# Optimization experiments

Measured on AMD Instinct MI355X. Metric: run time of the kernel, lower is better.

## Reference

```python
import jax, jax.numpy as jnp
import numpy as np

# static config matching init_kwargs
NODE, K, KER, STR = 32, 10, 5, 2
B, C = 8, 64
N = NODE * NODE          # 1024 nodes per sample
BN = B * N               # 8192 total nodes
OUT = (NODE - KER) // STR + 1
E = OUT * OUT            # local hyperedges per sample (196)
BN_EPS = 1e-5


def _local_block_diag():
    """Static block-diagonal local incidence matrix (BN, B*E), built once in numpy."""
    idx = np.arange(N).reshape(NODE, NODE)
    H_local = np.zeros((N, E), np.float32)
    e = 0
    for i in range(0, NODE - KER + 1, STR):
        for j in range(0, NODE - KER + 1, STR):
            H_local[idx[i:i + KER, j:j + KER].ravel(), e] = 1.0
            e += 1
    blk = np.zeros((BN, B * E), np.float32)
    for b in range(B):
        blk[b * N:(b + 1) * N, b * E:(b + 1) * E] = H_local
    return jnp.asarray(blk)


_LOCAL_BLK = _local_block_diag()


def setup_inputs() -> dict:
    key = jax.random.key(0)
    k1, k2 = jax.random.split(key, 2)
    x = jax.random.normal(k1, (B, N, C), jnp.float32)
    W_conv = jax.random.normal(k2, (C, C), jnp.float32) * 0.05
    b_conv = jnp.zeros((C,), jnp.float32)
    gamma = jnp.ones((C,), jnp.float32)
    beta = jnp.zeros((C,), jnp.float32)
    return {"x": x, "W_conv": W_conv, "b_conv": b_conv, "gamma": gamma, "beta": beta}


def reference(x, W_conv, b_conv, gamma, beta):
    xm = x.reshape(BN, C)                       # merged nodes (B*N, C)

    # --- hypergraph construction (no_grad in torch) ---
    xs = jax.lax.stop_gradient(xm)
    sq = jnp.sum(xs * xs, axis=-1, keepdims=True)
    dists = sq - 2.0 * (xs @ xs.T) + sq.T       # (BN, BN) pairwise sq-dists
    _, inds = jax.lax.top_k(-dists, K + 1)      # K+1 smallest distances
    # weights_function(prob=False) -> all ones; scatter incidence
    H = jnp.zeros((BN, BN), x.dtype).at[jnp.arange(BN)[:, None], inds].set(1.0)
    # Dv == K+1 for every row -> max_k = K+1 and the second topk gives new_H == H
    Hfull = jnp.concatenate([H, _LOCAL_BLK], axis=1)  # (BN, BN + B*E)

    # G = Dv^{-1/2} H W De^{-1} H^T Dv^{-1/2}, W = I, via diagonal scaling
    DV = Hfull.sum(axis=1)
    DE = jnp.maximum(Hfull.sum(axis=0), 1e-8)
    dv2 = DV ** -0.5
    A = dv2[:, None] * Hfull
    G = (A * (1.0 / DE)[None, :]) @ A.T          # (BN, BN)
    G = jax.lax.stop_gradient(G)

    # --- HGNN conv: linear -> G matmul -> BN (train stats) -> relu -> residual ---
    y = xm @ W_conv.T + b_conv                   # (BN, C)
    z = G @ y                                    # (BN, C)
    mu = z.mean(axis=0)
    var = z.var(axis=0)                          # biased, as torch BN training
    zn = (z - mu) / jnp.sqrt(var + BN_EPS) * gamma + beta
    out = jax.nn.relu(zn) + xm
    return out.reshape(B, N, C)
```

## Files before the change

kernel.cpp:

```cpp
#include <hip/hip_runtime.h>
#include <math.h>

#define BNTOT 8192
#define CH    64
#define KP1   11
#define NLOC  1568
#define MARGIN 1.0f
#define LCAPR 512

typedef __attribute__((ext_vector_type(8))) short short8;
typedef __attribute__((ext_vector_type(4))) float float4v;

__device__ __forceinline__ int pcnt(int p) {
  int lo = p - 4; if (lo < 0) lo = 0; lo += (lo & 1);
  int hi = p; if (hi > 26) hi = 26;
  return (hi >= lo) ? (((hi - lo) >> 1) + 1) : 0;
}
__device__ __forceinline__ float dv2_of(int u) {
  int node = u & 1023;
  int rr = node >> 5, cc = node & 31;
  int dv = KP1 + pcnt(rr) * pcnt(cc);
  return 1.0f / sqrtf((float)dv);
}
__device__ __forceinline__ unsigned short f2bf(float f) {
  unsigned u = __float_as_uint(f);
  unsigned r = (u + 0x7FFFu + ((u >> 16) & 1u)) >> 16;
  return (unsigned short)r;
}
__device__ __forceinline__ unsigned fkey(float s) {
  unsigned u = __float_as_uint(s);
  return (u & 0x80000000u) ? ~u : (u | 0x80000000u);
}
__device__ __forceinline__ unsigned long long skey(float s, int idx) {
  return ((unsigned long long)fkey(s) << 32) | (unsigned)idx;
}
__device__ __forceinline__ int mbcnt64(unsigned long long m) {
  return __builtin_amdgcn_mbcnt_hi((unsigned)(m >> 32),
         __builtin_amdgcn_mbcnt_lo((unsigned)m, 0));
}
__device__ __forceinline__ int wave_count4(int l) {
  return     __popcll(__ballot(l & 1))
       + 2 * __popcll(__ballot(l & 2))
       + 4 * __popcll(__ballot(l & 4))
       + 8 * __popcll(__ballot(l & 8));
}

__global__ void k_cast(const float* __restrict__ X, unsigned short* __restrict__ Xh,
                       float* __restrict__ sq) {
  int g = blockIdx.x * 256 + threadIdx.x;
  int lane = threadIdx.x & 63;
  float v = X[g];
  Xh[g] = f2bf(v);
  float s = v * v;
  #pragma unroll
  for (int off = 32; off >= 1; off >>= 1) s += __shfl_xor(s, off, 64);
  if (lane == 0) sq[g >> 6] = s;
}

__global__ __launch_bounds__(256)
void k_thrpart(const float* __restrict__ X, const float* __restrict__ sq,
               float* __restrict__ part) {
  const int tid = threadIdx.x, wave = tid >> 6, lane = tid & 63;
  const int rg = blockIdx.x >> 3, chunk = blockIdx.x & 7;
  const int row = rg * 64 + lane;
  float xr[CH];
  {
    const float4* xp = (const float4*)(X + (size_t)row * CH);
    #pragma unroll
    for (int k = 0; k < CH / 4; ++k) {
      float4 v = xp[k];
      xr[4*k+0] = v.x; xr[4*k+1] = v.y; xr[4*k+2] = v.z; xr[4*k+3] = v.w;
    }
  }
  float tv[KP1];
  #pragma unroll
  for (int t = 0; t < KP1; ++t) tv[t] = INFINITY;

  for (int s = 0; s < 32; ++s) {
    int j = __builtin_amdgcn_readfirstlane(((chunk * 4 + wave) * 32 + s) * 8);
    const float* cp = X + (size_t)j * CH;
    float d0 = 0.f, d1 = 0.f, d2 = 0.f, d3 = 0.f;
    #pragma unroll
    for (int k = 0; k < CH / 4; ++k) {
      d0 = fmaf(xr[4*k+0], cp[4*k+0], d0);
      d1 = fmaf(xr[4*k+1], cp[4*k+1], d1);
      d2 = fmaf(xr[4*k+2], cp[4*k+2], d2);
      d3 = fmaf(xr[4*k+3], cp[4*k+3], d3);
    }
    float cv = fmaf(-2.0f, (d0 + d1) + (d2 + d3), sq[j]);
    #pragma unroll
    for (int t = 0; t < KP1; ++t) {
      float lo = fminf(tv[t], cv), hi = fmaxf(tv[t], cv);
      tv[t] = lo; cv = hi;
    }
  }
  __shared__ float ls[4][64][KP1];
  #pragma unroll
  for (int t = 0; t < KP1; ++t) ls[wave][lane][t] = tv[t];
  __syncthreads();
  if (tid < 64) {
    float v[KP1];
    #pragma unroll
    for (int t = 0; t < KP1; ++t) v[t] = ls[0][tid][t];
    #pragma unroll
    for (int w = 1; w < 4; ++w)
      #pragma unroll
      for (int t = 0; t < KP1; ++t) {
        float cv = ls[w][tid][t];
        #pragma unroll
        for (int s2 = 0; s2 < KP1; ++s2) {
          float lo = fminf(v[s2], cv), hi = fmaxf(v[s2], cv);
          v[s2] = lo; cv = hi;
        }
      }
    size_t base = ((size_t)blockIdx.x * 64 + tid) * KP1;
    #pragma unroll
    for (int t = 0; t < KP1; ++t) part[base + t] = v[t];
  }
}

__global__ void k_thrmerge(const float* __restrict__ part, float* __restrict__ thr) {
  const int rg = blockIdx.x, lane = threadIdx.x;
  const int row = rg * 64 + lane;
  float v[KP1];
  {
    size_t b0 = ((size_t)(rg * 8) * 64 + lane) * KP1;
    #pragma unroll
    for (int t = 0; t < KP1; ++t) v[t] = part[b0 + t];
  }
  for (int c = 1; c < 8; ++c) {
    size_t b = ((size_t)(rg * 8 + c) * 64 + lane) * KP1;
    #pragma unroll
    for (int t = 0; t < KP1; ++t) {
      float cv = part[b + t];
      #pragma unroll
      for (int s2 = 0; s2 < KP1; ++s2) {
        float lo = fminf(v[s2], cv), hi = fmaxf(v[s2], cv);
        v[s2] = lo; cv = hi;
      }
    }
  }
  thr[row] = v[KP1 - 1] + MARGIN;
}

__global__ __launch_bounds__(256)
void k_filter(const unsigned short* __restrict__ Xh, const float* __restrict__ sq,
              const float* __restrict__ thr, unsigned long long* __restrict__ mask) {
  const int tid = threadIdx.x, wave = tid >> 6, lane = tid & 63;
  const int m = lane & 15, q = lane >> 4;
  const int rowbase = (blockIdx.x >> 5) * 64;
  const int colbase = (blockIdx.x & 31) * 256 + wave * 64;
  const int wcol = (blockIdx.x & 31) * 4 + wave;

  short8 a[4][2];
  #pragma unroll
  for (int rt = 0; rt < 4; ++rt)
    #pragma unroll
    for (int kc = 0; kc < 2; ++kc)
      a[rt][kc] = *(const short8*)(Xh + (size_t)(rowbase + rt * 16 + m) * CH + kc * 32 + q * 8);

  short8 b0[4], b1[4];
  float sqv[4];
  #pragma unroll
  for (int sub = 0; sub < 4; ++sub) {
    const int coln = colbase + sub * 16 + m;
    const short8* bp = (const short8*)(Xh + (size_t)coln * CH + q * 8);
    b0[sub] = bp[0];
    b1[sub] = bp[4];
    sqv[sub] = sq[coln];
  }

  float thrv[16];
  #pragma unroll
  for (int rt = 0; rt < 4; ++rt)
    #pragma unroll
    for (int r = 0; r < 4; ++r)
      thrv[rt * 4 + r] = thr[rowbase + rt * 16 + q * 4 + r];

  const float4v cz = {0.f, 0.f, 0.f, 0.f};
  const int sr = lane & 15, qq = sr >> 2, rr = sr & 3;

  #pragma unroll
  for (int rt = 0; rt < 4; ++rt) {
    unsigned long long bal[4][4];
    #pragma unroll
    for (int sub = 0; sub < 4; ++sub) {
      float4v c = __builtin_amdgcn_mfma_f32_16x16x32_bf16(a[rt][0], b0[sub], cz, 0, 0, 0);
      c = __builtin_amdgcn_mfma_f32_16x16x32_bf16(a[rt][1], b1[sub], c, 0, 0, 0);
      #pragma unroll
      for (int r = 0; r < 4; ++r) {
        float score = fmaf(-2.0f, c[r], sqv[sub]);
        bal[sub][r] = __ballot(score < thrv[rt * 4 + r]);
      }
    }
    unsigned long long w = 0;
    #pragma unroll
    for (int sub = 0; sub < 4; ++sub) {
      unsigned long long bsel = (rr == 0) ? bal[sub][0]
                              : (rr == 1) ? bal[sub][1]
                              : (rr == 2) ? bal[sub][2]
                              :             bal[sub][3];
      unsigned long long slice = (bsel >> (qq * 16)) & 0xFFFFull;
      w |= slice << (sub * 16);
    }
    if ((lane >> 4) == rt)
      mask[(size_t)(rowbase + rt * 16 + sr) * 128 + wcol] = w;
  }
}

__global__ __launch_bounds__(256)
void k_rescore(const float* __restrict__ X, const float* __restrict__ sq,
               const unsigned long long* __restrict__ mask,
               int* __restrict__ inds, int* __restrict__ DE) {
  __shared__ int cols[4][LCAPR];
  const int tid = threadIdx.x, lane = tid & 63, wv = tid >> 6;
  const int row = __builtin_amdgcn_readfirstlane(blockIdx.x * 4 + wv);

  float xr[CH];
  {
    const float4* xp = (const float4*)(X + (size_t)row * CH);
    #pragma unroll
    for (int k = 0; k < CH / 4; ++k) {
      float4 v = xp[k];
      xr[4*k+0] = v.x; xr[4*k+1] = v.y; xr[4*k+2] = v.z; xr[4*k+3] = v.w;
    }
  }

  const unsigned long long* mrow = mask + (size_t)row * 128;
  unsigned long long w0 = mrow[lane * 2 + 0];
  unsigned long long w1 = mrow[lane * 2 + 1];

  int cnt = __popcll(w0) + __popcll(w1);
  int p = 0, total = 0;
  #pragma unroll
  for (int b = 0; b < 8; ++b) {
    unsigned long long bb = __ballot((cnt >> b) & 1);
    p     += mbcnt64(bb) << b;
    total += __popcll(bb) << b;
  }

  if (total <= LCAPR) {
    unsigned long long w = w0;
    while (w) { int b = __builtin_ctzll(w); w &= w - 1; cols[wv][p++] = lane * 128 + b; }
    w = w1;
    while (w) { int b = __builtin_ctzll(w); w &= w - 1; cols[wv][p++] = lane * 128 + 64 + b; }

    unsigned kscore[8]; int kidx[8];
    #pragma unroll
    for (int a = 0; a < 8; ++a) { kscore[a] = 0xFFFFFFFFu; kidx[a] = 0; }
    #pragma unroll
    for (int a = 0; a < 8; ++a) {
      int s = a * 64 + lane;
      bool valid = s < total;
      int cj = cols[wv][valid ? s : 0];
      const float4* cp = (const float4*)(X + (size_t)cj * CH);
      float d0 = 0.f, d1 = 0.f, d2 = 0.f, d3 = 0.f;
      #pragma unroll
      for (int k = 0; k < CH / 4; ++k) {
        float4 v = cp[k];
        d0 = fmaf(xr[4*k+0], v.x, d0);
        d1 = fmaf(xr[4*k+1], v.y, d1);
        d2 = fmaf(xr[4*k+2], v.z, d2);
        d3 = fmaf(xr[4*k+3], v.w, d3);
      }
      float score = fmaf(-2.0f, (d0 + d1) + (d2 + d3), sq[cj]);
      if (valid) { kscore[a] = fkey(score); kidx[a] = cj; }
    }

    unsigned long long blo = 0, bhi = 1ull << 32;
    for (int it = 0; it < 32; ++it) {
      unsigned mid = (unsigned)((blo + bhi) >> 1);
      int l = 0;
      #pragma unroll
      for (int a = 0; a < 8; ++a) l += (kscore[a] < mid);
      if (wave_count4(l) < KP1) blo = mid; else bhi = mid;
    }
    const unsigned T = (unsigned)blo;

    int ll = 0, le = 0;
    #pragma unroll
    for (int a = 0; a < 8; ++a) { ll += (kscore[a] < T); le += (kscore[a] <= T); }
    int c_less = wave_count4(ll);
    int c_le   = wave_count4(le);
    const int needed = KP1 - c_less;
    const int cnt_eq = c_le - c_less;

    unsigned idxcut = BNTOT;
    if (cnt_eq != needed) {
      int lo2 = 0, hi2 = BNTOT;
      for (int it = 0; it < 13; ++it) {
        int mid2 = (lo2 + hi2) >> 1;
        int l2 = 0;
        #pragma unroll
        for (int a = 0; a < 8; ++a) l2 += ((kscore[a] == T) & (kidx[a] < mid2));
        if (wave_count4(l2) < needed) lo2 = mid2; else hi2 = mid2;
      }
      idxcut = (unsigned)hi2;
    }

    int base = 0;
    #pragma unroll
    for (int a = 0; a < 8; ++a) {
      bool win = (kscore[a] < T) | ((kscore[a] == T) & ((unsigned)kidx[a] < idxcut));
      unsigned long long bal = __ballot(win);
      int pos = base + mbcnt64(bal);
      if (win) {
        inds[(size_t)row * KP1 + pos] = kidx[a];
        atomicAdd(&DE[kidx[a]], 1);
      }
      base += __popcll(bal);
    }
  } else {
    float tv[KP1]; int ti[KP1];
    #pragma unroll
    for (int t = 0; t < KP1; ++t) { tv[t] = INFINITY; ti[t] = -1; }
    for (int s = lane; s < BNTOT; s += 64) {
      const float4* cp = (const float4*)(X + (size_t)s * CH);
      float d0 = 0.f, d1 = 0.f, d2 = 0.f, d3 = 0.f;
      #pragma unroll
      for (int k = 0; k < CH / 4; ++k) {
        float4 v = cp[k];
        d0 = fmaf(xr[4*k+0], v.x, d0);
        d1 = fmaf(xr[4*k+1], v.y, d1);
        d2 = fmaf(xr[4*k+2], v.z, d2);
        d3 = fmaf(xr[4*k+3], v.w, d3);
      }
      float score = fmaf(-2.0f, (d0 + d1) + (d2 + d3), sq[s]);
      if (score < tv[KP1 - 1]) {
        float cv = score; int ci = s;
        #pragma unroll
        for (int t = 0; t < KP1; ++t) {
          bool sw = cv < tv[t];
          float nv = sw ? cv    : tv[t]; int ni = sw ? ci    : ti[t];
          float ov = sw ? tv[t] : cv;    int oi = sw ? ti[t] : ci;
          tv[t] = nv; ti[t] = ni; cv = ov; ci = oi;
        }
      }
    }
    unsigned long long cur = skey(tv[0], ti[0]);
    unsigned long long keep = 0;
    #pragma unroll
    for (int t = 0; t < KP1; ++t) {
      unsigned long long mw = cur;
      #pragma unroll
      for (int off = 1; off < 64; off <<= 1) {
        unsigned lo = __shfl_xor((unsigned)mw, off, 64);
        unsigned hi = __shfl_xor((unsigned)(mw >> 32), off, 64);
        unsigned long long o = ((unsigned long long)hi << 32) | lo;
        mw = (o < mw) ? o : mw;
      }
      if (lane == t) keep = mw;
      if (cur == mw) {
        #pragma unroll
        for (int q = 0; q < KP1 - 1; ++q) { tv[q] = tv[q+1]; ti[q] = ti[q+1]; }
        tv[KP1-1] = INFINITY; ti[KP1-1] = -1;
        cur = skey(tv[0], ti[0]);
      }
    }
    if (lane < KP1) {
      int idx = (int)(unsigned)(keep & 0xFFFFFFFFull);
      inds[(size_t)row * KP1 + lane] = idx;
      atomicAdd(&DE[idx], 1);
    }
  }
}

__global__ void k_lin(const float* __restrict__ X, const float* __restrict__ W,
                      const float* __restrict__ bias, float* __restrict__ t) {
  int lane = threadIdx.x & 63;
  int wave = threadIdx.x >> 6;
  int rowbase = (blockIdx.x * 4 + wave) * 4;
  float wr[CH];
  {
    const float4* wp = (const float4*)(W + (size_t)lane * CH);
    #pragma unroll
    for (int k = 0; k < CH / 4; ++k) {
      float4 v = wp[k];
      wr[4*k+0] = v.x; wr[4*k+1] = v.y; wr[4*k+2] = v.z; wr[4*k+3] = v.w;
    }
  }
  float bc = bias[lane];
  #pragma unroll
  for (int r = 0; r < 4; ++r) {
    int row = __builtin_amdgcn_readfirstlane(rowbase + r);
    const float* xp = X + (size_t)row * CH;
    float d0 = 0.f, d1 = 0.f, d2 = 0.f, d3 = 0.f;
    #pragma unroll
    for (int k = 0; k < CH / 4; ++k) {
      d0 = fmaf(wr[4*k+0], xp[4*k+0], d0);
      d1 = fmaf(wr[4*k+1], xp[4*k+1], d1);
      d2 = fmaf(wr[4*k+2], xp[4*k+2], d2);
      d3 = fmaf(wr[4*k+3], xp[4*k+3], d3);
    }
    float y = (d0 + d1) + (d2 + d3) + bc;
    t[(size_t)row * CH + lane] = y * dv2_of(row);
  }
}

__global__ void k_edge(const float* __restrict__ t, const int* __restrict__ inds,
                       float* __restrict__ s_knn, float* __restrict__ s_loc) {
  int c = threadIdx.x & 63;
  int w = threadIdx.x >> 6;
  if (blockIdx.x < BNTOT / 4) {
    int u = blockIdx.x * 4 + w;
    float val = t[(size_t)u * CH + c];
    int ub = __builtin_amdgcn_readfirstlane(u);
    const int* ip = inds + (size_t)ub * KP1;
    #pragma unroll
    for (int j = 0; j < KP1; ++j) {
      int e = ip[j];
      atomicAdd(&s_knn[(size_t)e * CH + c], val);
    }
  } else {
    int e = (blockIdx.x - BNTOT / 4) * 4 + w;
    int b  = e / 196;
    int le = e - b * 196;
    int pi = le / 14;
    int pj = le - pi * 14;
    int base = b * 1024 + (pi * 2) * 32 + pj * 2;
    float acc = 0.f;
    #pragma unroll
    for (int di = 0; di < 5; ++di)
      #pragma unroll
      for (int dj = 0; dj < 5; ++dj)
        acc += t[(size_t)(base + di * 32 + dj) * CH + c];
    s_loc[(size_t)e * CH + c] = acc * (1.0f / 25.0f);
  }
}

__global__ void k_gatherbn(const float* __restrict__ s_knn, const float* __restrict__ s_loc,
                           const int* __restrict__ inds, const int* __restrict__ DE,
                           float* __restrict__ z, float* __restrict__ gsum,
                           float* __restrict__ gsumsq) {
  int c = threadIdx.x & 63;
  int w = threadIdx.x >> 6;
  int u = blockIdx.x * 4 + w;
  int ub = __builtin_amdgcn_readfirstlane(u);
  const int* ip = inds + (size_t)ub * KP1;
  float acc = 0.f;
  #pragma unroll
  for (int j = 0; j < KP1; ++j) {
    int e = ip[j];
    float invde = 1.0f / (float)DE[e];
    acc += s_knn[(size_t)e * CH + c] * invde;
  }
  int node = ub & 1023, b = ub >> 10;
  int rr = node >> 5, cc = node & 31;
  int i0 = rr - 4; if (i0 < 0) i0 = 0; i0 += (i0 & 1);
  int i1 = rr; if (i1 > 26) i1 = 26;
  int j0 = cc - 4; if (j0 < 0) j0 = 0; j0 += (j0 & 1);
  int j1 = cc; if (j1 > 26) j1 = 26;
  for (int i = i0; i <= i1; i += 2)
    for (int jj = j0; jj <= j1; jj += 2) {
      int e = b * 196 + (i >> 1) * 14 + (jj >> 1);
      acc += s_loc[(size_t)e * CH + c];
    }
  float zv = acc * dv2_of(ub);
  z[(size_t)ub * CH + c] = zv;

  __shared__ float ls[4][CH], ls2[4][CH];
  ls[w][c] = zv; ls2[w][c] = zv * zv;
  __syncthreads();
  if (threadIdx.x < 64) {
    int bin = (blockIdx.x & 7) * CH;
    atomicAdd(&gsum[bin + c],   ls[0][c] + ls[1][c] + ls[2][c] + ls[3][c]);
    atomicAdd(&gsumsq[bin + c], ls2[0][c] + ls2[1][c] + ls2[2][c] + ls2[3][c]);
  }
}

__global__ void k_out(const float* __restrict__ z, const float* __restrict__ X,
                      const float* __restrict__ gsum, const float* __restrict__ gsumsq,
                      const float* __restrict__ gamma, const float* __restrict__ beta,
                      float* __restrict__ out) {
  int c = threadIdx.x & 63;
  int w = threadIdx.x >> 6;
  float S = 0.f, S2 = 0.f;
  #pragma unroll
  for (int b = 0; b < 8; ++b) {
    S  += gsum[b * CH + c];
    S2 += gsumsq[b * CH + c];
  }
  float m = S * (1.0f / (float)BNTOT);
  float var = S2 * (1.0f / (float)BNTOT) - m * m;
  float rstd = 1.0f / sqrtf(var + 1e-5f);

  int u = blockIdx.x * 4 + w;
  size_t idx = (size_t)u * CH + c;
  float zn = (z[idx] - m) * rstd * gamma[c] + beta[c];
  out[idx] = fmaxf(zn, 0.f) + X[idx];
}

extern "C" void kernel_launch(void* const* d_in, const int* in_sizes, int n_in,
                              void* d_out, int out_size, void* d_ws, size_t ws_size,
                              hipStream_t stream) {
  const float* X     = (const float*)d_in[0];
  const float* W     = (const float*)d_in[1];
  const float* bias  = (const float*)d_in[2];
  const float* gamma = (const float*)d_in[3];
  const float* beta  = (const float*)d_in[4];
  float* out = (float*)d_out;

  float* ws = (float*)d_ws;
  float* sq      = ws;
  float* thr     = sq + 8192;
  float* t       = thr + 8192;
  float* s_loc   = t + 524288;
  float* z       = s_loc + 100352;
  float* thrpart = z + 524288;
  int*   inds    = (int*)(thrpart + 720896);
  unsigned short* Xh = (unsigned short*)(inds + 90112);
  unsigned long long* mask = (unsigned long long*)(Xh + 524288);
  int*   DE     = (int*)(mask + (size_t)8192 * 128);
  float* gsum   = (float*)(DE + 8192);
  float* gsumsq = gsum + 512;
  float* s_knn  = gsumsq + 512;

  hipMemsetAsync(DE, 0, (size_t)(8192 + 512 + 512 + 524288) * 4, stream);

  k_cast    <<<2048, 256, 0, stream>>>(X, Xh, sq);
  k_thrpart <<<1024, 256, 0, stream>>>(X, sq, thrpart);
  k_thrmerge<<<128, 64, 0, stream>>>(thrpart, thr);
  k_filter  <<<4096, 256, 0, stream>>>(Xh, sq, thr, mask);
  k_rescore <<<2048, 256, 0, stream>>>(X, sq, mask, inds, DE);
  k_lin     <<<512, 256, 0, stream>>>(X, W, bias, t);
  k_edge    <<<BNTOT / 4 + NLOC / 4, 256, 0, stream>>>(t, inds, s_knn, s_loc);
  k_gatherbn<<<BNTOT / 4, 256, 0, stream>>>(s_knn, s_loc, inds, DE, z, gsum, gsumsq);
  k_out     <<<BNTOT / 4, 256, 0, stream>>>(z, X, gsum, gsumsq, gamma, beta, out);

  (void)in_sizes; (void)n_in; (void)out_size; (void)ws_size;
}
```

Before: 240.5 us.

## Rescore candidates with 16-lane cooperative dot products and DPP reductions

The fast path of the rescoring kernel no longer has each lane compute a full 64-channel dot product against its own candidate from a 64-float register copy of the query row. Each group of 16 lanes now loads coalesced float4 slices, and cross-lane DPP adds reduce the partial sums, so four candidates are scored per step. This cuts register pressure and spreads memory access across lanes. The candidate cap drops from 512 to 256, and the full-row fallback (now holding the query in registers only there) handles more rows, which costs more if many rows exceed 256 candidates.

```diff
diff --git a/kernel.cpp b/kernel.cpp
--- a/kernel.cpp
+++ b/kernel.cpp
@@ -6,7 +6,7 @@
 #define KP1   11
 #define NLOC  1568
 #define MARGIN 1.0f
-#define LCAPR 512
+#define LCAPR 256
 
 typedef __attribute__((ext_vector_type(8))) short short8;
 typedef __attribute__((ext_vector_type(4))) float float4v;
@@ -43,6 +43,11 @@
        + 2 * __popcll(__ballot(l & 2))
        + 4 * __popcll(__ballot(l & 4))
        + 8 * __popcll(__ballot(l & 8));
+}
+template <int CTRL>
+__device__ __forceinline__ float dpp_add(float x) {
+  int p = __builtin_amdgcn_update_dpp(0, __float_as_int(x), CTRL, 0xF, 0xF, true);
+  return x + __int_as_float(p);
 }
 
 __global__ void k_cast(const float* __restrict__ X, unsigned short* __restrict__ Xh,
@@ -214,17 +219,7 @@
                int* __restrict__ inds, int* __restrict__ DE) {
   __shared__ int cols[4][LCAPR];
   const int tid = threadIdx.x, lane = tid & 63, wv = tid >> 6;
-  const int row = __builtin_amdgcn_readfirstlane(blockIdx.x * 4 + wv);
-
-  float xr[CH];
-  {
-    const float4* xp = (const float4*)(X + (size_t)row * CH);
-    #pragma unroll
-    for (int k = 0; k < CH / 4; ++k) {
-      float4 v = xp[k];
-      xr[4*k+0] = v.x; xr[4*k+1] = v.y; xr[4*k+2] = v.z; xr[4*k+3] = v.w;
-    }
-  }
+  const int row = __builtin_amdgcn_readfirstlane(blockIdx.x * 4 + (tid >> 6));
 
   const unsigned long long* mrow = mask + (size_t)row * 128;
   unsigned long long w0 = mrow[lane * 2 + 0];
@@ -245,26 +240,32 @@
     w = w1;
     while (w) { int b = __builtin_ctzll(w); w &= w - 1; cols[wv][p++] = lane * 128 + 64 + b; }
 
-    unsigned kscore[8]; int kidx[8];
-    #pragma unroll
-    for (int a = 0; a < 8; ++a) { kscore[a] = 0xFFFFFFFFu; kidx[a] = 0; }
-    #pragma unroll
-    for (int a = 0; a < 8; ++a) {
-      int s = a * 64 + lane;
-      bool valid = s < total;
-      int cj = cols[wv][valid ? s : 0];
-      const float4* cp = (const float4*)(X + (size_t)cj * CH);
-      float d0 = 0.f, d1 = 0.f, d2 = 0.f, d3 = 0.f;
-      #pragma unroll
-      for (int k = 0; k < CH / 4; ++k) {
-        float4 v = cp[k];
-        d0 = fmaf(xr[4*k+0], v.x, d0);
-        d1 = fmaf(xr[4*k+1], v.y, d1);
-        d2 = fmaf(xr[4*k+2], v.z, d2);
-        d3 = fmaf(xr[4*k+3], v.w, d3);
-      }
-      float score = fmaf(-2.0f, (d0 + d1) + (d2 + d3), sq[cj]);
-      if (valid) { kscore[a] = fkey(score); kidx[a] = cj; }
+    const int m = lane & 15, q = lane >> 4;
+    const float4 xrv = *(const float4*)(X + (size_t)row * CH + m * 4);
+
+    unsigned kscore[4]; int kidx[4];
+    #pragma unroll
+    for (int a = 0; a < 4; ++a) { kscore[a] = 0xFFFFFFFFu; kidx[a] = 0; }
+
+    #pragma unroll
+    for (int slot = 0; slot < 4; ++slot) {
+      if (slot * 64 < total) {
+        #pragma unroll
+        for (int b = 0; b < 16; ++b) {
+          int s = slot * 64 + b * 4 + q;
+          bool valid = s < total;
+          int sc = valid ? s : (total - 1);
+          int cj = cols[wv][sc];
+          const float4 v = *(const float4*)(X + (size_t)cj * CH + m * 4);
+          float d = fmaf(xrv.x, v.x, fmaf(xrv.y, v.y, fmaf(xrv.z, v.z, xrv.w * v.w)));
+          d = dpp_add<0xB1>(d);
+          d = dpp_add<0x4E>(d);
+          d = dpp_add<0x141>(d);
+          d = dpp_add<0x140>(d);
+          float score = fmaf(-2.0f, d, sq[cj]);
+          if (valid && m == b) { kscore[slot] = fkey(score); kidx[slot] = cj; }
+        }
+      }
     }
 
     unsigned long long blo = 0, bhi = 1ull << 32;
@@ -272,14 +273,14 @@
       unsigned mid = (unsigned)((blo + bhi) >> 1);
       int l = 0;
       #pragma unroll
-      for (int a = 0; a < 8; ++a) l += (kscore[a] < mid);
+      for (int a = 0; a < 4; ++a) l += (kscore[a] < mid);
       if (wave_count4(l) < KP1) blo = mid; else bhi = mid;
     }
     const unsigned T = (unsigned)blo;
 
     int ll = 0, le = 0;
     #pragma unroll
-    for (int a = 0; a < 8; ++a) { ll += (kscore[a] < T); le += (kscore[a] <= T); }
+    for (int a = 0; a < 4; ++a) { ll += (kscore[a] < T); le += (kscore[a] <= T); }
     int c_less = wave_count4(ll);
     int c_le   = wave_count4(le);
     const int needed = KP1 - c_less;
@@ -292,7 +293,7 @@
         int mid2 = (lo2 + hi2) >> 1;
         int l2 = 0;
         #pragma unroll
-        for (int a = 0; a < 8; ++a) l2 += ((kscore[a] == T) & (kidx[a] < mid2));
+        for (int a = 0; a < 4; ++a) l2 += ((kscore[a] == T) & (kidx[a] < mid2));
         if (wave_count4(l2) < needed) lo2 = mid2; else hi2 = mid2;
       }
       idxcut = (unsigned)hi2;
@@ -300,7 +301,7 @@
 
     int base = 0;
     #pragma unroll
-    for (int a = 0; a < 8; ++a) {
+    for (int a = 0; a < 4; ++a) {
       bool win = (kscore[a] < T) | ((kscore[a] == T) & ((unsigned)kidx[a] < idxcut));
       unsigned long long bal = __ballot(win);
       int pos = base + mbcnt64(bal);
@@ -311,6 +312,15 @@
       base += __popcll(bal);
     }
   } else {
+    float xr[CH];
+    {
+      const float4* xp = (const float4*)(X + (size_t)row * CH);
+      #pragma unroll
+      for (int k = 0; k < CH / 4; ++k) {
+        float4 v = xp[k];
+        xr[4*k+0] = v.x; xr[4*k+1] = v.y; xr[4*k+2] = v.z; xr[4*k+3] = v.w;
+      }
+    }
     float tv[KP1]; int ti[KP1];
     #pragma unroll
     for (int t = 0; t < KP1; ++t) { tv[t] = INFINITY; ti[t] = -1; }
@@ -352,7 +362,7 @@
       if (lane == t) keep = mw;
       if (cur == mw) {
         #pragma unroll
-        for (int q = 0; q < KP1 - 1; ++q) { tv[q] = tv[q+1]; ti[q] = ti[q+1]; }
+        for (int q2 = 0; q2 < KP1 - 1; ++q2) { tv[q2] = tv[q2+1]; ti[q2] = ti[q2+1]; }
         tv[KP1-1] = INFINITY; ti[KP1-1] = -1;
         cur = skey(tv[0], ti[0]);
       }
```

After: 250.6 us. 4.2% more time.

## Split each rescore row across four waves and merge per-wave top-K in shared memory

Applied to the files above, without the earlier changes.

k_rescore now assigns one block per row, with each of the four waves handling a quarter of the candidate bitmask (2048 columns). Each wave selects its local top-11 by a threshold binary search, writes the keys to shared memory, and wave 0 then merges the 44 candidates to the final top-11. The goal is to raise parallelism and cut the per-wave serial work (fewer candidate slots per lane, and a per-quarter fallback scan instead of a full 8192-column scan). The cost is four times as many blocks, a block-wide barrier and an extra merge step, and the per-wave capacity is lower (128), so the slow fallback path may trigger more often.

```diff
diff --git a/kernel.cpp b/kernel.cpp
--- a/kernel.cpp
+++ b/kernel.cpp
@@ -6,7 +6,7 @@
 #define KP1   11
 #define NLOC  1568
 #define MARGIN 1.0f
-#define LCAPR 512
+#define LCAPW 128
 
 typedef __attribute__((ext_vector_type(8))) short short8;
 typedef __attribute__((ext_vector_type(4))) float float4v;
@@ -31,12 +31,13 @@
   unsigned u = __float_as_uint(s);
   return (u & 0x80000000u) ? ~u : (u | 0x80000000u);
 }
-__device__ __forceinline__ unsigned long long skey(float s, int idx) {
-  return ((unsigned long long)fkey(s) << 32) | (unsigned)idx;
-}
 __device__ __forceinline__ int mbcnt64(unsigned long long m) {
   return __builtin_amdgcn_mbcnt_hi((unsigned)(m >> 32),
          __builtin_amdgcn_mbcnt_lo((unsigned)m, 0));
+}
+__device__ __forceinline__ int wave_count2(int l) {
+  return     __popcll(__ballot(l & 1))
+       + 2 * __popcll(__ballot(l & 2));
 }
 __device__ __forceinline__ int wave_count4(int l) {
   return     __popcll(__ballot(l & 1))
@@ -210,11 +211,12 @@
 
 __global__ __launch_bounds__(256)
 void k_rescore(const float* __restrict__ X, const float* __restrict__ sq,
-               const unsigned long long* __restrict__ mask,
+               const unsigned* __restrict__ mask32,
                int* __restrict__ inds, int* __restrict__ DE) {
-  __shared__ int cols[4][LCAPR];
+  __shared__ int cols[4][LCAPW];
+  __shared__ unsigned long long wkeys[4 * KP1];
   const int tid = threadIdx.x, lane = tid & 63, wv = tid >> 6;
-  const int row = __builtin_amdgcn_readfirstlane(blockIdx.x * 4 + wv);
+  const int row = blockIdx.x;
 
   float xr[CH];
   {
@@ -226,95 +228,80 @@
     }
   }
 
-  const unsigned long long* mrow = mask + (size_t)row * 128;
-  unsigned long long w0 = mrow[lane * 2 + 0];
-  unsigned long long w1 = mrow[lane * 2 + 1];
-
-  int cnt = __popcll(w0) + __popcll(w1);
-  int p = 0, total = 0;
-  #pragma unroll
-  for (int b = 0; b < 8; ++b) {
+  unsigned wbits = mask32[(size_t)row * 256 + wv * 64 + lane];
+  int cnt = __popc(wbits);
+  int p = 0, subtotal = 0;
+  #pragma unroll
+  for (int b = 0; b < 6; ++b) {
     unsigned long long bb = __ballot((cnt >> b) & 1);
-    p     += mbcnt64(bb) << b;
-    total += __popcll(bb) << b;
-  }
-
-  if (total <= LCAPR) {
-    unsigned long long w = w0;
-    while (w) { int b = __builtin_ctzll(w); w &= w - 1; cols[wv][p++] = lane * 128 + b; }
-    w = w1;
-    while (w) { int b = __builtin_ctzll(w); w &= w - 1; cols[wv][p++] = lane * 128 + 64 + b; }
-
-    unsigned kscore[8]; int kidx[8];
-    #pragma unroll
-    for (int a = 0; a < 8; ++a) { kscore[a] = 0xFFFFFFFFu; kidx[a] = 0; }
-    #pragma unroll
-    for (int a = 0; a < 8; ++a) {
-      int s = a * 64 + lane;
-      bool valid = s < total;
-      int cj = cols[wv][valid ? s : 0];
-      const float4* cp = (const float4*)(X + (size_t)cj * CH);
-      float d0 = 0.f, d1 = 0.f, d2 = 0.f, d3 = 0.f;
-      #pragma unroll
-      for (int k = 0; k < CH / 4; ++k) {
-        float4 v = cp[k];
-        d0 = fmaf(xr[4*k+0], v.x, d0);
-        d1 = fmaf(xr[4*k+1], v.y, d1);
-        d2 = fmaf(xr[4*k+2], v.z, d2);
-        d3 = fmaf(xr[4*k+3], v.w, d3);
-      }
-      float score = fmaf(-2.0f, (d0 + d1) + (d2 + d3), sq[cj]);
-      if (valid) { kscore[a] = fkey(score); kidx[a] = cj; }
+    p        += mbcnt64(bb) << b;
+    subtotal += __popcll(bb) << b;
+  }
+
+  if (subtotal <= LCAPW) {
+    const int cbase = wv * 2048 + lane * 32;
+    unsigned w = wbits;
+    while (w) { int b = __builtin_ctz(w); w &= w - 1; cols[wv][p++] = cbase + b; }
+
+    unsigned ks[2]; int ki[2];
+    ks[0] = ks[1] = 0xFFFFFFFFu; ki[0] = lane; ki[1] = 64 + lane;
+    #pragma unroll
+    for (int a = 0; a < 2; ++a) {
+      if (a * 64 < subtotal) {
+        int s = a * 64 + lane;
+        bool valid = s < subtotal;
+        int cj = cols[wv][valid ? s : (subtotal - 1)];
+        const float4* cp = (const float4*)(X + (size_t)cj * CH);
+        float d0 = 0.f, d1 = 0.f, d2 = 0.f, d3 = 0.f;
+        #pragma unroll
+        for (int k = 0; k < CH / 4; ++k) {
+          float4 v = cp[k];
+          d0 = fmaf(xr[4*k+0], v.x, d0);
+          d1 = fmaf(xr[4*k+1], v.y, d1);
+          d2 = fmaf(xr[4*k+2], v.z, d2);
+          d3 = fmaf(xr[4*k+3], v.w, d3);
+        }
+        float score = fmaf(-2.0f, (d0 + d1) + (d2 + d3), sq[cj]);
+        if (valid) { ks[a] = fkey(score); ki[a] = cj; }
+      }
     }
 
     unsigned long long blo = 0, bhi = 1ull << 32;
     for (int it = 0; it < 32; ++it) {
       unsigned mid = (unsigned)((blo + bhi) >> 1);
-      int l = 0;
-      #pragma unroll
-      for (int a = 0; a < 8; ++a) l += (kscore[a] < mid);
-      if (wave_count4(l) < KP1) blo = mid; else bhi = mid;
+      int l = (ks[0] < mid) + (ks[1] < mid);
+      if (wave_count2(l) < KP1) blo = mid; else bhi = mid;
     }
     const unsigned T = (unsigned)blo;
-
-    int ll = 0, le = 0;
-    #pragma unroll
-    for (int a = 0; a < 8; ++a) { ll += (kscore[a] < T); le += (kscore[a] <= T); }
-    int c_less = wave_count4(ll);
-    int c_le   = wave_count4(le);
-    const int needed = KP1 - c_less;
-    const int cnt_eq = c_le - c_less;
-
-    unsigned idxcut = BNTOT;
+    int ll = (ks[0] < T) + (ks[1] < T);
+    int le = (ks[0] <= T) + (ks[1] <= T);
+    int c_less = wave_count2(ll), c_le = wave_count2(le);
+    const int needed = KP1 - c_less, cnt_eq = c_le - c_less;
+    unsigned idxcut = 0xFFFFFFFFu;
     if (cnt_eq != needed) {
       int lo2 = 0, hi2 = BNTOT;
       for (int it = 0; it < 13; ++it) {
         int mid2 = (lo2 + hi2) >> 1;
-        int l2 = 0;
-        #pragma unroll
-        for (int a = 0; a < 8; ++a) l2 += ((kscore[a] == T) & (kidx[a] < mid2));
-        if (wave_count4(l2) < needed) lo2 = mid2; else hi2 = mid2;
+        int l2 = ((ks[0] == T) & (ki[0] < mid2)) + ((ks[1] == T) & (ki[1] < mid2));
+        if (wave_count2(l2) < needed) lo2 = mid2; else hi2 = mid2;
       }
       idxcut = (unsigned)hi2;
     }
-
     int base = 0;
     #pragma unroll
-    for (int a = 0; a < 8; ++a) {
-      bool win = (kscore[a] < T) | ((kscore[a] == T) & ((unsigned)kidx[a] < idxcut));
+    for (int a = 0; a < 2; ++a) {
+      bool win = (ks[a] < T) | ((ks[a] == T) & ((unsigned)ki[a] < idxcut));
       unsigned long long bal = __ballot(win);
       int pos = base + mbcnt64(bal);
-      if (win) {
-        inds[(size_t)row * KP1 + pos] = kidx[a];
-        atomicAdd(&DE[kidx[a]], 1);
-      }
+      if (win && pos < KP1)
+        wkeys[wv * KP1 + pos] = ((unsigned long long)ks[a] << 32) | (unsigned)ki[a];
       base += __popcll(bal);
     }
   } else {
     float tv[KP1]; int ti[KP1];
     #pragma unroll
     for (int t = 0; t < KP1; ++t) { tv[t] = INFINITY; ti[t] = -1; }
-    for (int s = lane; s < BNTOT; s += 64) {
+    for (int s = wv * 2048 + lane; s < (wv + 1) * 2048; s += 64) {
       const float4* cp = (const float4*)(X + (size_t)s * CH);
       float d0 = 0.f, d1 = 0.f, d2 = 0.f, d3 = 0.f;
       #pragma unroll
@@ -331,36 +318,86 @@
         #pragma unroll
         for (int t = 0; t < KP1; ++t) {
           bool sw = cv < tv[t];
-          float nv = sw ? cv    : tv[t]; int ni = sw ? ci    : ti[t];
+          float nv = sw ? cv    : tv[t]; int ni = sw ? ti[t] : ti[t];
+          ni = sw ? ci : ti[t];
           float ov = sw ? tv[t] : cv;    int oi = sw ? ti[t] : ci;
           tv[t] = nv; ti[t] = ni; cv = ov; ci = oi;
         }
       }
     }
-    unsigned long long cur = skey(tv[0], ti[0]);
-    unsigned long long keep = 0;
+    unsigned kk[KP1];
+    #pragma unroll
+    for (int t = 0; t < KP1; ++t) kk[t] = fkey(tv[t]);
+    unsigned long long blo = 0, bhi = 1ull << 32;
+    for (int it = 0; it < 32; ++it) {
+      unsigned mid = (unsigned)((blo + bhi) >> 1);
+      int l = 0;
+      #pragma unroll
+      for (int t = 0; t < KP1; ++t) l += (kk[t] < mid);
+      if (wave_count4(l) < KP1) blo = mid; else bhi = mid;
+    }
+    const unsigned T = (unsigned)blo;
+    int ll = 0, le = 0;
+    #pragma unroll
+    for (int t = 0; t < KP1; ++t) { ll += (kk[t] < T); le += (kk[t] <= T); }
+    int c_less = wave_count4(ll), c_le = wave_count4(le);
+    const int needed = KP1 - c_less, cnt_eq = c_le - c_less;
+    unsigned idxcut = 0xFFFFFFFFu;
+    if (cnt_eq != needed) {
+      int lo2 = 0, hi2 = BNTOT;
+      for (int it = 0; it < 13; ++it) {
+        int mid2 = (lo2 + hi2) >> 1;
+        int l2 = 0;
+        #pragma unroll
+        for (int t = 0; t < KP1; ++t) l2 += ((kk[t] == T) & (ti[t] < mid2));
+        if (wave_count4(l2) < needed) lo2 = mid2; else hi2 = mid2;
+      }
+      idxcut = (unsigned)hi2;
+    }
+    int base = 0;
     #pragma unroll
     for (int t = 0; t < KP1; ++t) {
-      unsigned long long mw = cur;
-      #pragma unroll
-      for (int off = 1; off < 64; off <<= 1) {
-        unsigned lo = __shfl_xor((unsigned)mw, off, 64);
-        unsigned hi = __shfl_xor((unsigned)(mw >> 32), off, 64);
-        unsigned long long o = ((unsigned long long)hi << 32) | lo;
-        mw = (o < mw) ? o : mw;
-      }
-      if (lane == t) keep = mw;
-      if (cur == mw) {
-        #pragma unroll
-        for (int q = 0; q < KP1 - 1; ++q) { tv[q] = tv[q+1]; ti[q] = ti[q+1]; }
-        tv[KP1-1] = INFINITY; ti[KP1-1] = -1;
-        cur = skey(tv[0], ti[0]);
-      }
-    }
-    if (lane < KP1) {
-      int idx = (int)(unsigned)(keep & 0xFFFFFFFFull);
-      inds[(size_t)row * KP1 + lane] = idx;
-      atomicAdd(&DE[idx], 1);
+      bool win = (kk[t] < T) | ((kk[t] == T) & ((unsigned)ti[t] < idxcut));
+      unsigned long long bal = __ballot(win);
+      int pos = base + mbcnt64(bal);
+      if (win && pos < KP1)
+        wkeys[wv * KP1 + pos] = ((unsigned long long)kk[t] << 32) | (unsigned)ti[t];
+      base += __popcll(bal);
+    }
+  }
+
+  __syncthreads();
+
+  if (wv == 0) {
+    unsigned long long key = (lane < 4 * KP1) ? wkeys[lane] : ~0ull;
+    unsigned kss = (unsigned)(key >> 32);
+    unsigned kii = (unsigned)(key & 0xFFFFFFFFull);
+    unsigned long long blo = 0, bhi = 1ull << 32;
+    for (int it = 0; it < 32; ++it) {
+      unsigned mid = (unsigned)((blo + bhi) >> 1);
+      int c = __popcll(__ballot(kss < mid));
+      if (c < KP1) blo = mid; else bhi = mid;
+    }
+    const unsigned Tm = (unsigned)blo;
+    int c_less = __popcll(__ballot(kss < Tm));
+    int c_le   = __popcll(__ballot(kss <= Tm));
+    const int needed = KP1 - c_less, cnt_eq = c_le - c_less;
+    unsigned idxc = 0xFFFFFFFFu;
+    if (cnt_eq != needed) {
+      int lo2 = 0, hi2 = BNTOT;
+      for (int it = 0; it < 13; ++it) {
+        int mid2 = (lo2 + hi2) >> 1;
+        int c2 = __popcll(__ballot((kss == Tm) & ((int)kii < mid2)));
+        if (c2 < needed) lo2 = mid2; else hi2 = mid2;
+      }
+      idxc = (unsigned)hi2;
+    }
+    bool win = (kss < Tm) | ((kss == Tm) & (kii < idxc));
+    unsigned long long bal = __ballot(win);
+    int pos = mbcnt64(bal);
+    if (win && pos < KP1) {
+      inds[(size_t)row * KP1 + pos] = (int)kii;
+      atomicAdd(&DE[(int)kii], 1);
     }
   }
 }
@@ -521,7 +558,7 @@
   k_thrpart <<<1024, 256, 0, stream>>>(X, sq, thrpart);
   k_thrmerge<<<128, 64, 0, stream>>>(thrpart, thr);
   k_filter  <<<4096, 256, 0, stream>>>(Xh, sq, thr, mask);
-  k_rescore <<<2048, 256, 0, stream>>>(X, sq, mask, inds, DE);
+  k_rescore <<<BNTOT, 256, 0, stream>>>(X, sq, (const unsigned*)mask, inds, DE);
   k_lin     <<<512, 256, 0, stream>>>(X, W, bias, t);
   k_edge    <<<BNTOT / 4 + NLOC / 4, 256, 0, stream>>>(t, inds, s_knn, s_loc);
   k_gatherbn<<<BNTOT / 4, 256, 0, stream>>>(s_knn, s_loc, inds, DE, z, gsum, gsumsq);
```

Measured after the change: 249.6 us. 1.04x slower.
